# Kernel optimization log

Measured on AMD Instinct MI355X. Metric: run time of the kernel, lower is better.

## Reference

```python
import jax, jax.numpy as jnp
import numpy as np

N_PIX = 596   # (151-2)*(6-2) after two VALID 2x2 convs
HEADS, D = 4, 64

def _ln(x, axes, g=None, b=None, eps=1e-5):
    mu = jnp.mean(x, axes, keepdims=True)
    var = jnp.var(x, axes, keepdims=True)
    y = (x - mu) * jax.lax.rsqrt(var + eps)
    return y * g + b if g is not None else y

def _conv(x, w, b):
    y = jax.lax.conv_general_dilated(x, w, (1, 1), 'VALID',
                                     dimension_numbers=('NCHW', 'OIHW', 'NCHW'))
    return y + b[None, :, None, None]


def setup_inputs() -> dict:
    key = jax.random.key(0)
    ks = jax.random.split(key, 24)
    f32 = jnp.float32
    w = lambda k, s: jax.random.normal(k, s, f32) * 0.05
    inp = {
        'x': jax.random.normal(ks[0], (64, 4, 151, 6), f32),
        'conv1_w': w(ks[1], (16, 4, 2, 2)),  'conv1_b': w(ks[2], (16,)),
        'conv2_w': w(ks[3], (32, 16, 2, 2)), 'conv2_b': w(ks[4], (32,)),
        'kp_w': w(ks[5], (34, 256)),  'kp_b': w(ks[6], (256,)),
        'qp_w': w(ks[7], (34, 256)),  'qp_b': w(ks[8], (256,)),
        'vp_w': w(ks[9], (34, 256)),  'vp_b': w(ks[10], (256,)),
        'klin_w': w(ks[11], (64, N_PIX)), 'klin_b': w(ks[12], (N_PIX,)),
        'qlin_w': w(ks[13], (64, N_PIX)), 'qlin_b': w(ks[14], (N_PIX,)),
        'alin_w': w(ks[15], (N_PIX, N_PIX)), 'alin_b': w(ks[16], (N_PIX,)),
        'knorm_g': jnp.ones((HEADS, N_PIX, D), f32), 'knorm_b': jnp.zeros((HEADS, N_PIX, D), f32),
        'qnorm_g': jnp.ones((HEADS, N_PIX, D), f32), 'qnorm_b': jnp.zeros((HEADS, N_PIX, D), f32),
        'vnorm_g': jnp.ones((HEADS, N_PIX, D), f32), 'vnorm_b': jnp.zeros((HEADS, N_PIX, D), f32),
        'lin1_w': w(ks[17], (256, 64)), 'lin1_b': w(ks[18], (64,)),
        'lin2_w': w(ks[19], (64, 10)),  'lin2_b': w(ks[20], (10,)),
    }
    return inp


def reference(x, conv1_w, conv1_b, conv2_w, conv2_b,
              kp_w, kp_b, qp_w, qp_b, vp_w, vp_b,
              klin_w, klin_b, qlin_w, qlin_b, alin_w, alin_b,
              knorm_g, knorm_b, qnorm_g, qnorm_b, vnorm_g, vnorm_b,
              lin1_w, lin1_b, lin2_w, lin2_b):
    h = jax.nn.relu(_conv(x, conv1_w, conv1_b))
    h = jax.nn.relu(_conv(h, conv2_w, conv2_b))          # (N,32,149,4)
    N, C, cH, cW = h.shape
    xc = jnp.broadcast_to(jnp.arange(cW, dtype=h.dtype) / cW, (cH, cW))
    yc = jnp.broadcast_to((jnp.arange(cH, dtype=h.dtype) / cH)[:, None], (cH, cW))
    sp = jnp.broadcast_to(jnp.stack([xc, yc])[None], (N, 2, cH, cW))
    feats = jnp.concatenate([h, sp], axis=1).transpose(0, 2, 3, 1).reshape(N, N_PIX, C + 2)
    proj = lambda w_, b_: (feats @ w_ + b_).reshape(N, N_PIX, HEADS, D).transpose(0, 2, 1, 3)
    K = _ln(proj(kp_w, kp_b), (1, 2, 3), knorm_g, knorm_b)   # (N,h,596,64)
    Q = _ln(proj(qp_w, qp_b), (1, 2, 3), qnorm_g, qnorm_b)
    V = _ln(proj(vp_w, vp_b), (1, 2, 3), vnorm_g, vnorm_b)
    A = jax.nn.elu((Q @ qlin_w + qlin_b) + (K @ klin_w + klin_b))  # (N,h,596,596)
    A = jax.nn.softmax(A @ alin_w + alin_b, axis=-1)
    E = jnp.einsum('bhfc,bhcd->bhfd', A, V)                  # (N,h,596,64)
    E = E.transpose(0, 2, 1, 3).reshape(N, N_PIX, HEADS * D)
    E = jax.nn.relu(E @ lin1_w + lin1_b)
    E = _ln(E, (1, 2))                                       # LN over [596,64], no affine
    E = jnp.max(E, axis=1)                                   # (N,64)
    return jax.nn.elu(E @ lin2_w + lin2_b)                   # (N,10)
```

## Files before the change

### kernel.cpp

```cpp
#include <hip/hip_runtime.h>
#include <hip/hip_bf16.h>
#include <math.h>

typedef __hip_bfloat16 bf16;
typedef unsigned short ushort;
typedef __attribute__((ext_vector_type(8))) short short8;
typedef __attribute__((ext_vector_type(4))) float float4v;

#define BATCH 64
#define NPIX 596
#define CH 34
#define PC 256

static __device__ __forceinline__ ushort f2bu(float v){ bf16 h = __float2bfloat16(v); return *(ushort*)&h; }
static __device__ __forceinline__ float bu2f(ushort u){ bf16 h = *(bf16*)&u; return __bfloat162float(h); }
static __device__ __forceinline__ float eluf(float x){ return x > 0.f ? x : expm1f(x); }

__global__ __launch_bounds__(256) void k_conv_feats(
    const float* __restrict__ x,
    const float* __restrict__ w1, const float* __restrict__ b1,
    const float* __restrict__ w2, const float* __restrict__ b2,
    ushort* __restrict__ featsH, ushort* __restrict__ featsL)
{
  __shared__ float sw1[256];
  __shared__ float sb1[16];
  __shared__ float sw2[2048];
  __shared__ float sb2[32];
  __shared__ float h1[16*20*5];
  const int s = blockIdx.x, b = blockIdx.y, t = threadIdx.x;
  const float* xb = x + (size_t)b * 4*151*6;

  const int p0 = s*75;
  const int p1 = (p0+75 < NPIX) ? p0+75 : NPIX;
  const int rA = p0>>2, rB = (p1-1)>>2;
  const int nh = rB - rA + 2;

  sw1[t]=w1[t];
  if (t<16) sb1[t]=b1[t];
  for (int i=t;i<2048;i+=256) sw2[i]=w2[i];
  if (t<32) sb2[t]=b2[t];
  __syncthreads();

  for (int i=t; i<16*nh*5; i+=256){
    int oc = i/(nh*5), rem = i - oc*(nh*5);
    int lr = rem/5, cc = rem - (rem/5)*5;
    int r = rA + lr;
    float acc = sb1[oc];
    #pragma unroll
    for (int ic=0;ic<4;ic++){
      const float* xp = xb + ic*906 + r*6 + cc;
      const float* wp = sw1 + oc*16 + ic*4;
      acc += xp[0]*wp[0] + xp[1]*wp[1] + xp[6]*wp[2] + xp[7]*wp[3];
    }
    h1[(oc*20 + lr)*5 + cc] = fmaxf(acc, 0.f);
  }
  __syncthreads();

  const int np = p1 - p0;
  ushort* fbH = featsH + (size_t)b*NPIX*64;
  ushort* fbL = featsL + (size_t)b*NPIX*64;
  const short8 z8 = {0,0,0,0,0,0,0,0};
  for (int i=t;i<np*4;i+=256){
    int pl = i>>2, off = 32 + (i&3)*8;
    int p = p0 + pl;
    *(short8*)(fbH + (size_t)p*64 + off) = z8;
    *(short8*)(fbL + (size_t)p*64 + off) = z8;
  }
  for (int i=t;i<32*np;i+=256){
    int oc = i/np, pl = i - oc*np;
    int p = p0 + pl;
    int r = p>>2, cc = p&3;
    int lr = r - rA;
    float acc = sb2[oc];
    #pragma unroll
    for (int ic=0;ic<16;ic++){
      const float* hp = h1 + (ic*20 + lr)*5 + cc;
      const float* wp = sw2 + oc*64 + ic*4;
      acc += hp[0]*wp[0] + hp[1]*wp[1] + hp[5]*wp[2] + hp[6]*wp[3];
    }
    float v = fmaxf(acc, 0.f);
    ushort hu = f2bu(v);
    fbH[(size_t)p*64+oc] = hu;
    fbL[(size_t)p*64+oc] = f2bu(v - bu2f(hu));
  }
  __syncthreads();
  for (int pl=t; pl<np; pl+=256){
    int p = p0 + pl;
    float v1 = (float)(p&3)*0.25f;
    float v2 = (float)(p>>2)*(1.0f/149.0f);
    ushort h1u = f2bu(v1), h2u = f2bu(v2);
    fbH[(size_t)p*64+32] = h1u;  fbL[(size_t)p*64+32] = f2bu(v1 - bu2f(h1u));
    fbH[(size_t)p*64+33] = h2u;  fbL[(size_t)p*64+33] = f2bu(v2 - bu2f(h2u));
  }
}

__global__ __launch_bounds__(256) void k_prep(
    const float* __restrict__ aw, const float* __restrict__ qw, const float* __restrict__ kw,
    const float* __restrict__ l1w,
    const float* __restrict__ kpw, const float* __restrict__ qpw, const float* __restrict__ vpw,
    ushort* __restrict__ alinP, ushort* __restrict__ WqkP, ushort* __restrict__ w1T,
    ushort* __restrict__ projP)
{
  __shared__ float sA[4][32][17];
  const int t = threadIdx.x, w = t>>6, l = t&63;
  const int gw = blockIdx.x*4 + w;

  if (gw < 1016){
    const float* src; ushort* dst;
    int row0, col0, nrow, ncol, rstride; size_t slot;
    if (gw < 760){
      int tile = gw/19, kk = gw - tile*19;
      src = aw; rstride = NPIX; nrow = NPIX; ncol = NPIX;
      row0 = kk*32; col0 = tile*16;
      dst = alinP; slot = (size_t)gw*64;
    } else if (gw < 920){
      int g1 = gw - 760;
      int tile = g1>>2, kk = g1&3;
      rstride = NPIX; nrow = 64; ncol = NPIX;
      col0 = tile*16;
      if (kk < 2){ src = qw; row0 = kk*32; }
      else       { src = kw; row0 = (kk-2)*32; }
      dst = WqkP; slot = (size_t)g1*64;
    } else {
      int g2 = gw - 920;
      int which = g2>>5, rem = g2&31;
      int tile = rem>>1, kk = rem&1;
      src = which==0 ? kpw : which==1 ? qpw : vpw;
      rstride = PC; nrow = CH; ncol = PC;
      row0 = kk*32; col0 = tile*16;
      dst = projP; slot = (size_t)g2*64;
    }
    #pragma unroll
    for (int p=0;p<2;p++){
      int rr = p*16 + (l>>2);
      int r = row0 + rr;
      int cb = (l&3)*4;
      #pragma unroll
      for (int j=0;j<4;j++){
        int c = col0 + cb + j;
        float v = (r < nrow && c < ncol) ? src[(size_t)r*rstride + c] : 0.f;
        sA[w][rr][cb + j] = v;
      }
    }
    __syncthreads();
    int nloc = l&15, c0 = (l>>4)*8;
    ushort out[8];
    #pragma unroll
    for (int i=0;i<8;i++) out[i] = f2bu(sA[w][c0+i][nloc]);
    *(short8*)(dst + (slot + l)*8) = *(short8*)out;
  } else {
    int s3 = (gw - 1016)*64 + l;
    int n = s3>>5, e0 = (s3&31)*8;
    ushort out[8];
    #pragma unroll
    for (int i=0;i<8;i++) out[i] = f2bu(l1w[(size_t)(e0+i)*64 + n]);
    *(short8*)(w1T + (size_t)s3*8) = *(short8*)out;
  }
}

__global__ __launch_bounds__(256) void k_proj_p1(
    const ushort* __restrict__ featsH, const ushort* __restrict__ featsL,
    const ushort* __restrict__ projP,
    const float* __restrict__ kpb, const float* __restrict__ qpb, const float* __restrict__ vpb,
    float* __restrict__ statsP)
{
  __shared__ float red[8];
  const int rb = blockIdx.x, b = blockIdx.y, which = blockIdx.z;
  const int t = threadIdx.x, w = t>>6, l = t&63, quad = l>>4, ln = l&15;
  const float* Bv = which==0 ? kpb : which==1 ? qpb : vpb;

  float4v acc[4][4];
  #pragma unroll
  for (int ms=0;ms<4;ms++)
    #pragma unroll
    for (int i=0;i<4;i++) acc[ms][i] = (float4v){0.f,0.f,0.f,0.f};

  #pragma unroll
  for (int kk=0;kk<4;kk++){
    const ushort* fb = (kk<2 ? featsH : featsL) + (size_t)b*NPIX*64;
    short8 aq[4];
    #pragma unroll
    for (int ms=0;ms<4;ms++){
      int r = rb*64 + ms*16 + ln;
      short8 z = {0,0,0,0,0,0,0,0};
      aq[ms] = (r < NPIX) ? *(const short8*)(fb + (size_t)r*64 + (kk&1)*32 + quad*8) : z;
    }
    #pragma unroll
    for (int i=0;i<4;i++){
      int tile = w + 4*i;
      short8 bf = *(const short8*)(projP + ((size_t)((which*16 + tile)*2 + (kk&1))*64 + l)*8);
      #pragma unroll
      for (int ms=0;ms<4;ms++)
        acc[ms][i] = __builtin_amdgcn_mfma_f32_16x16x32_bf16(aq[ms], bf, acc[ms][i], 0,0,0);
    }
  }
  float s=0.f, s2=0.f;
  #pragma unroll
  for (int i=0;i<4;i++){
    int col = (w+4*i)*16 + ln;
    float bc = Bv[col];
    #pragma unroll
    for (int ms=0;ms<4;ms++)
      #pragma unroll
      for (int r=0;r<4;r++){
        int p = rb*64 + ms*16 + quad*4 + r;
        if (p < NPIX){
          float v = acc[ms][i][r] + bc;
          s += v; s2 += v*v;
        }
      }
  }
  #pragma unroll
  for (int o=32;o>0;o>>=1){ s += __shfl_down(s,o); s2 += __shfl_down(s2,o); }
  if (l==0){ red[w]=s; red[4+w]=s2; }
  __syncthreads();
  if (t==0){
    atomicAdd(&statsP[(which*64+b)*2],   red[0]+red[1]+red[2]+red[3]);
    atomicAdd(&statsP[(which*64+b)*2+1], red[4]+red[5]+red[6]+red[7]);
  }
}

__global__ __launch_bounds__(256) void k_proj_p2(
    const ushort* __restrict__ featsH, const ushort* __restrict__ featsL,
    const ushort* __restrict__ projP,
    const float* __restrict__ kpb, const float* __restrict__ qpb, const float* __restrict__ vpb,
    const float* __restrict__ kg, const float* __restrict__ kb_,
    const float* __restrict__ qg, const float* __restrict__ qb_,
    const float* __restrict__ vg, const float* __restrict__ vb_,
    const float* __restrict__ statsP,
    ushort* __restrict__ Kb, ushort* __restrict__ Qb, ushort* __restrict__ VP)
{
  __shared__ ushort vtile[64*264];
  const int rb = blockIdx.x, b = blockIdx.y, which = blockIdx.z;
  const int t = threadIdx.x, w = t>>6, l = t&63, quad = l>>4, ln = l&15;
  const float* Bv = which==0 ? kpb : which==1 ? qpb : vpb;
  const float* G  = which==0 ? kg  : which==1 ? qg  : vg;
  const float* Be = which==0 ? kb_ : which==1 ? qb_ : vb_;

  float4v acc[4][4];
  #pragma unroll
  for (int ms=0;ms<4;ms++)
    #pragma unroll
    for (int i=0;i<4;i++) acc[ms][i] = (float4v){0.f,0.f,0.f,0.f};

  #pragma unroll
  for (int kk=0;kk<4;kk++){
    const ushort* fb = (kk<2 ? featsH : featsL) + (size_t)b*NPIX*64;
    short8 aq[4];
    #pragma unroll
    for (int ms=0;ms<4;ms++){
      int r = rb*64 + ms*16 + ln;
      short8 z = {0,0,0,0,0,0,0,0};
      aq[ms] = (r < NPIX) ? *(const short8*)(fb + (size_t)r*64 + (kk&1)*32 + quad*8) : z;
    }
    #pragma unroll
    for (int i=0;i<4;i++){
      int tile = w + 4*i;
      short8 bf = *(const short8*)(projP + ((size_t)((which*16 + tile)*2 + (kk&1))*64 + l)*8);
      #pragma unroll
      for (int ms=0;ms<4;ms++)
        acc[ms][i] = __builtin_amdgcn_mfma_f32_16x16x32_bf16(aq[ms], bf, acc[ms][i], 0,0,0);
    }
  }
  const float n = (float)(NPIX*PC);
  const float S  = statsP[(which*64+b)*2];
  const float S2 = statsP[(which*64+b)*2+1];
  const float mu = S/n;
  const float rs = rsqrtf(S2/n - mu*mu + 1e-5f);

  if (which < 2){
    ushort* out = which==0 ? Kb : Qb;
    #pragma unroll
    for (int i=0;i<4;i++){
      int col = (w+4*i)*16 + ln;
      int h = col>>6, d = col&63;
      float bc = Bv[col];
      #pragma unroll
      for (int ms=0;ms<4;ms++)
        #pragma unroll
        for (int r=0;r<4;r++){
          int p = rb*64 + ms*16 + quad*4 + r;
          if (p < NPIX){
            int gi = (h*NPIX+p)*64 + d;
            float y = (acc[ms][i][r] + bc - mu)*rs*G[gi] + Be[gi];
            out[((size_t)(b*4+h)*NPIX + p)*64 + d] = f2bu(y);
          }
        }
    }
  } else {
    #pragma unroll
    for (int i=0;i<4;i++){
      int col = (w+4*i)*16 + ln;
      int h = col>>6, d = col&63;
      float bc = Bv[col];
      #pragma unroll
      for (int ms=0;ms<4;ms++)
        #pragma unroll
        for (int r=0;r<4;r++){
          int lrow = ms*16 + quad*4 + r;
          int p = rb*64 + lrow;
          ushort o = 0;
          if (p < NPIX){
            int gi = (h*NPIX+p)*64 + d;
            o = f2bu((acc[ms][i][r] + bc - mu)*rs*G[gi] + Be[gi]);
          }
          vtile[lrow*264 + col] = o;
        }
    }
    __syncthreads();
    #pragma unroll
    for (int e=0;e<8;e++){
      int sid = e*256 + t;
      int l2 = sid & 63;
      int rest = sid >> 6;
      int kkL = rest & 1, w2 = (rest>>1)&3, hh = rest>>3;
      int kk = rb*2 + kkL;
      if (kk < 19){
        int lrow0 = kkL*32 + ((l2>>4)<<3);
        int col = hh*64 + w2*16 + (l2&15);
        ushort o[8];
        #pragma unroll
        for (int jj=0;jj<8;jj++) o[jj] = vtile[(lrow0+jj)*264 + col];
        *(short8*)(VP + ((size_t)(b*4+hh)*4864 + (w2*19 + kk)*64 + l2)*8) = *(short8*)o;
      }
    }
  }
}

__global__ __launch_bounds__(512, 2) void k_attn(
    const ushort* __restrict__ Qb, const ushort* __restrict__ Kb,
    const ushort* __restrict__ alinP, const ushort* __restrict__ WqkP,
    const ushort* __restrict__ VP,
    const float* __restrict__ qbias, const float* __restrict__ kbias,
    const float* __restrict__ abias,
    ushort* __restrict__ Ew)
{
  extern __shared__ __align__(16) ushort sm[];
  ushort* strip = sm;
  float*  red   = (float*)(sm + 78848);
  float*  rsum  = (float*)(sm + 78848 + 2048);

  const int t = threadIdx.x;
  const int w = t>>6, l = t&63, quad = l>>4, ln = l&15;
  const int id  = blockIdx.x + blockIdx.y*5;
  const int xcd = id & 7, idx = id >> 3;
  const int lin = xcd*160 + idx;
  const int bh  = lin/5, rb = lin - bh*5;
  const int b = bh>>2, h = bh&3;
  const int row0 = rb*128;
  const ushort* Qp = Qb + (size_t)bh*NPIX*64;
  const ushort* Kp = Kb + (size_t)bh*NPIX*64;

  float4v acc[8][5];
  #pragma unroll
  for (int ms=0;ms<8;ms++)
    #pragma unroll
    for (int i=0;i<5;i++) acc[ms][i] = (float4v){0.f,0.f,0.f,0.f};

  #pragma unroll
  for (int kk=0;kk<4;kk++){
    short8 aq[8];
    #pragma unroll
    for (int ms=0;ms<8;ms++){
      int r = row0 + ms*16 + ln;
      short8 z = {0,0,0,0,0,0,0,0};
      aq[ms] = (r < NPIX)
        ? *(const short8*)((kk<2 ? Qp : Kp) + (size_t)r*64 + (kk&1)*32 + quad*8) : z;
    }
    __builtin_amdgcn_s_setprio(1);
    #pragma unroll
    for (int i=0;i<5;i++){
      int tile = w + 8*i;
      short8 bf = *(const short8*)(WqkP + ((size_t)(tile*4 + kk)*64 + l)*8);
      #pragma unroll
      for (int ms=0;ms<8;ms++)
        acc[ms][i] = __builtin_amdgcn_mfma_f32_16x16x32_bf16(aq[ms], bf, acc[ms][i], 0,0,0);
    }
    __builtin_amdgcn_s_setprio(0);
  }
  #pragma unroll
  for (int i=0;i<5;i++){
    int t0 = w + 8*i;
    if (t0 < 38){
      int col = t0*16 + ln;
      bool cv = col < NPIX;
      float qkb = cv ? (qbias[col] + kbias[col]) : 0.f;
      #pragma unroll
      for (int ms=0;ms<8;ms++)
        #pragma unroll
        for (int r=0;r<4;r++){
          float v = 0.f;
          if (cv){ float xx = acc[ms][i][r] + qkb; v = xx > 0.f ? xx : __expf(xx) - 1.f; }
          strip[(ms*16+quad*4+r)*616 + col] = f2bu(v);
        }
    }
  }
  __syncthreads();

  #pragma unroll
  for (int ms=0;ms<8;ms++)
    #pragma unroll
    for (int i=0;i<5;i++) acc[ms][i] = (float4v){0.f,0.f,0.f,0.f};
  for (int kk=0;kk<19;kk++){
    short8 af[8];
    #pragma unroll
    for (int ms=0;ms<8;ms++)
      af[ms] = *(const short8*)(strip + (ms*16+ln)*616 + kk*32 + quad*8);
    __builtin_amdgcn_s_setprio(1);
    #pragma unroll
    for (int i=0;i<5;i++){
      int tile = w + 8*i;
      short8 bf = *(const short8*)(alinP + ((size_t)(tile*19 + kk)*64 + l)*8);
      #pragma unroll
      for (int ms=0;ms<8;ms++)
        acc[ms][i] = __builtin_amdgcn_mfma_f32_16x16x32_bf16(af[ms], bf, acc[ms][i], 0,0,0);
    }
    __builtin_amdgcn_s_setprio(0);
  }
  __syncthreads();

  float sum[8][4];
  #pragma unroll
  for (int ms=0;ms<8;ms++)
    #pragma unroll
    for (int r=0;r<4;r++) sum[ms][r] = 0.f;
  #pragma unroll
  for (int i=0;i<5;i++){
    int t0 = w + 8*i;
    if (t0 < 38){
      int col = t0*16 + ln;
      bool cv = col < NPIX;
      float ab = cv ? abias[col] : 0.f;
      #pragma unroll
      for (int ms=0;ms<8;ms++)
        #pragma unroll
        for (int r=0;r<4;r++){
          float e = cv ? __expf(acc[ms][i][r] + ab) : 0.f;
          sum[ms][r] += e;
          strip[(ms*16+quad*4+r)*616 + col] = f2bu(e);
        }
    }
  }
  #pragma unroll
  for (int ms=0;ms<8;ms++)
    #pragma unroll
    for (int r=0;r<4;r++)
      #pragma unroll
      for (int o=8;o>0;o>>=1) sum[ms][r] += __shfl_xor(sum[ms][r], o, 16);
  if (ln==0){
    #pragma unroll
    for (int ms=0;ms<8;ms++)
      #pragma unroll
      for (int r=0;r<4;r++) red[(ms*16+quad*4+r)*8 + w] = sum[ms][r];
  }
  __syncthreads();
  if (t < 128){
    float4v v0 = *(float4v*)&red[t*8];
    float4v v1 = *(float4v*)&red[t*8+4];
    rsum[t] = (v0[0]+v0[1]+v0[2]+v0[3]) + (v1[0]+v1[1]+v1[2]+v1[3]);
  }
  __syncthreads();

  const int wr = w>>2, wc = w&3;
  float4v ve[4];
  #pragma unroll
  for (int ms=0;ms<4;ms++) ve[ms] = (float4v){0.f,0.f,0.f,0.f};
  for (int kk=0;kk<19;kk++){
    short8 bf = *(const short8*)(VP + ((size_t)bh*4864 + (wc*19 + kk)*64 + l)*8);
    __builtin_amdgcn_s_setprio(1);
    #pragma unroll
    for (int ms=0;ms<4;ms++){
      short8 af = *(const short8*)(strip + (wr*64 + ms*16+ln)*616 + kk*32 + quad*8);
      ve[ms] = __builtin_amdgcn_mfma_f32_16x16x32_bf16(af, bf, ve[ms], 0,0,0);
    }
    __builtin_amdgcn_s_setprio(0);
  }
  #pragma unroll
  for (int ms=0;ms<4;ms++)
    #pragma unroll
    for (int r=0;r<4;r++){
      int lrow = wr*64 + ms*16 + quad*4 + r;
      int p = row0 + lrow;
      if (p < NPIX){
        float inv = 1.f / rsum[lrow];
        Ew[((size_t)b*NPIX + p)*256 + h*64 + wc*16 + ln] = f2bu(ve[ms][r] * inv);
      }
    }
}

__global__ __launch_bounds__(256) void k_lin1(
    const ushort* __restrict__ Ew, const ushort* __restrict__ w1T,
    const float* __restrict__ bias,
    float* __restrict__ colmax, float* __restrict__ stats)
{
  __shared__ ushort sw1[64*264];
  __shared__ float red[8];
  const int t = threadIdx.x;
  const int w = t>>6, l = t&63, quad = l>>4, ln = l&15;
  const int rb = blockIdx.x, b = blockIdx.y;
  for (int g=t; g<2048; g+=256){
    int row = g>>5, q = g&31;
    *(short8*)(sw1 + row*264 + q*8) = *(const short8*)(w1T + row*256 + q*8);
  }
  __syncthreads();
  float4v acc[4];
  #pragma unroll
  for (int ms=0;ms<4;ms++) acc[ms] = (float4v){0.f,0.f,0.f,0.f};
  #pragma unroll
  for (int kk=0;kk<8;kk++){
    short8 bf = *(const short8*)(sw1 + (w*16+ln)*264 + kk*32 + quad*8);
    #pragma unroll
    for (int ms=0;ms<4;ms++){
      int p = rb*64 + ms*16 + ln;
      size_t rowi = (size_t)b*NPIX + (p < NPIX ? p : 0);
      short8 a = *(const short8*)(Ew + rowi*256 + kk*32 + quad*8);
      acc[ms] = __builtin_amdgcn_mfma_f32_16x16x32_bf16(a, bf, acc[ms], 0,0,0);
    }
  }
  const int col = w*16 + ln;
  const float bc = bias[col];
  float s=0.f, s2=0.f, cmx=0.f;
  #pragma unroll
  for (int ms=0;ms<4;ms++)
    #pragma unroll
    for (int r=0;r<4;r++){
      int p = rb*64 + ms*16 + quad*4 + r;
      if (p < NPIX){
        float v = fmaxf(acc[ms][r] + bc, 0.f);
        s += v; s2 += v*v;
        cmx = fmaxf(cmx, v);
      }
    }
  cmx = fmaxf(cmx, __shfl_xor(cmx, 16, 64));
  cmx = fmaxf(cmx, __shfl_xor(cmx, 32, 64));
  if (quad == 0)
    atomicMax((int*)&colmax[b*64 + col], __float_as_int(cmx));
  #pragma unroll
  for (int o=32;o>0;o>>=1){ s += __shfl_down(s,o); s2 += __shfl_down(s2,o); }
  if (l==0){ red[w]=s; red[4+w]=s2; }
  __syncthreads();
  if (t==0){
    atomicAdd(&stats[b*2],   red[0]+red[1]+red[2]+red[3]);
    atomicAdd(&stats[b*2+1], red[4]+red[5]+red[6]+red[7]);
  }
}

__global__ __launch_bounds__(64) void k_final(
    const float* __restrict__ colmax, const float* __restrict__ stats,
    const float* __restrict__ w2, const float* __restrict__ b2v,
    float* __restrict__ out)
{
  __shared__ float nm[64];
  const int b = blockIdx.x, t = threadIdx.x;
  {
    float mm = colmax[b*64 + t];
    const float n = (float)(NPIX*64);
    float S = stats[b*2], S2 = stats[b*2+1];
    float mu = S/n, var = S2/n - mu*mu;
    nm[t] = (mm - mu) * rsqrtf(var + 1e-5f);
  }
  __syncthreads();
  if (t<10){
    float acc = b2v[t];
    for (int e=0;e<64;e++) acc += nm[e]*w2[e*10+t];
    out[b*10+t] = eluf(acc);
  }
}

extern "C" void kernel_launch(void* const* d_in, const int* in_sizes, int n_in,
                              void* d_out, int out_size, void* d_ws, size_t ws_size,
                              hipStream_t stream)
{
  const float* x       = (const float*)d_in[0];
  const float* conv1_w = (const float*)d_in[1];
  const float* conv1_b = (const float*)d_in[2];
  const float* conv2_w = (const float*)d_in[3];
  const float* conv2_b = (const float*)d_in[4];
  const float* kp_w    = (const float*)d_in[5];
  const float* kp_b    = (const float*)d_in[6];
  const float* qp_w    = (const float*)d_in[7];
  const float* qp_b    = (const float*)d_in[8];
  const float* vp_w    = (const float*)d_in[9];
  const float* vp_b    = (const float*)d_in[10];
  const float* klin_w  = (const float*)d_in[11];
  const float* klin_b  = (const float*)d_in[12];
  const float* qlin_w  = (const float*)d_in[13];
  const float* qlin_b  = (const float*)d_in[14];
  const float* alin_w  = (const float*)d_in[15];
  const float* alin_b  = (const float*)d_in[16];
  const float* knorm_g = (const float*)d_in[17];
  const float* knorm_b = (const float*)d_in[18];
  const float* qnorm_g = (const float*)d_in[19];
  const float* qnorm_b = (const float*)d_in[20];
  const float* vnorm_g = (const float*)d_in[21];
  const float* vnorm_b = (const float*)d_in[22];
  const float* lin1_w  = (const float*)d_in[23];
  const float* lin1_b  = (const float*)d_in[24];
  const float* lin2_w  = (const float*)d_in[25];
  const float* lin2_b  = (const float*)d_in[26];

  float* feats  = (float*)d_ws;
  float* F      = feats + (size_t)BATCH*NPIX*CH;
  float* statsE = F + (size_t)BATCH*NPIX*64;
  float* statsP = statsE + 128;
  float* colmax = statsP + 384;
  ushort* Qb    = (ushort*)(colmax + 4096);
  ushort* Kb    = Qb + (size_t)BATCH*4*NPIX*64;
  ushort* Vb    = Kb + (size_t)BATCH*4*NPIX*64;
  ushort* Ew    = Vb + (size_t)BATCH*4*NPIX*64;
  ushort* w1T   = Ew + (size_t)BATCH*NPIX*256;
  ushort* alinP = w1T + 16384;
  ushort* WqkP  = alinP + 389120;
  ushort* VP    = WqkP + 81920;
  ushort* projP = VP + 9961472;
  ushort* featsH = (ushort*)feats;
  ushort* featsL = (ushort*)F;

  hipMemsetAsync(statsE, 0, 4608*sizeof(float), stream);

  dim3 gc(8, BATCH);
  k_conv_feats<<<gc, 256, 0, stream>>>(x, conv1_w, conv1_b, conv2_w, conv2_b, featsH, featsL);

  k_prep<<<262, 256, 0, stream>>>(alin_w, qlin_w, klin_w, lin1_w, kp_w, qp_w, vp_w,
                                  alinP, WqkP, w1T, projP);

  dim3 gp(10, BATCH, 3);
  k_proj_p1<<<gp, 256, 0, stream>>>(featsH, featsL, projP, kp_b, qp_b, vp_b, statsP);
  k_proj_p2<<<gp, 256, 0, stream>>>(featsH, featsL, projP, kp_b, qp_b, vp_b,
                                    knorm_g, knorm_b, qnorm_g, qnorm_b, vnorm_g, vnorm_b,
                                    statsP, Kb, Qb, VP);

  static bool attr_set = false;
  if (!attr_set){
    hipFuncSetAttribute((const void*)k_attn, hipFuncAttributeMaxDynamicSharedMemorySize, 162304);
    attr_set = true;
  }

  dim3 ga(5, BATCH*4);
  k_attn<<<ga, 512, 162304, stream>>>(Qb, Kb, alinP, WqkP, VP,
                                      qlin_b, klin_b, alin_b, Ew);

  dim3 gl(10, BATCH);
  k_lin1<<<gl, 256, 0, stream>>>(Ew, w1T, lin1_b, colmax, statsE);

  k_final<<<BATCH, 64, 0, stream>>>(colmax, statsE, lin2_w, lin2_b, (float*)d_out);
}
```

Before: 523.7 us.

## Compute projection LayerNorm stats via feature Gram matrix instead of extra GEMM pass

Removes the first projection pass that recomputed the full 596x256 projections only to get sum and sum-of-squares for LayerNorm. Instead the conv kernel accumulates a per-batch 34x34 Gram matrix and feature sums, a few extra prep blocks compute W^T W, weight row sums and bias terms, and a small kernel combines them into the mean and variance statistics. This trades a GEMM-sized pass for tiny reductions. The risk is fp32 cancellation in the variance formula and extra atomics in the conv kernel.

```diff
diff --git a/kernel.cpp b/kernel.cpp
--- a/kernel.cpp
+++ b/kernel.cpp
@@ -20,13 +20,15 @@
     const float* __restrict__ x,
     const float* __restrict__ w1, const float* __restrict__ b1,
     const float* __restrict__ w2, const float* __restrict__ b2,
-    ushort* __restrict__ featsH, ushort* __restrict__ featsL)
+    ushort* __restrict__ featsH, ushort* __restrict__ featsL,
+    float* __restrict__ Gbuf, float* __restrict__ sfb)
 {
   __shared__ float sw1[256];
   __shared__ float sb1[16];
   __shared__ float sw2[2048];
   __shared__ float sb2[32];
   __shared__ float h1[16*20*5];
+  __shared__ float fle[75*34];
   const int s = blockIdx.x, b = blockIdx.y, t = threadIdx.x;
   const float* xb = x + (size_t)b * 4*151*6;
 
@@ -82,8 +84,8 @@
     ushort hu = f2bu(v);
     fbH[(size_t)p*64+oc] = hu;
     fbL[(size_t)p*64+oc] = f2bu(v - bu2f(hu));
-  }
-  __syncthreads();
+    fle[pl*34+oc] = v;
+  }
   for (int pl=t; pl<np; pl+=256){
     int p = p0 + pl;
     float v1 = (float)(p&3)*0.25f;
@@ -91,6 +93,20 @@
     ushort h1u = f2bu(v1), h2u = f2bu(v2);
     fbH[(size_t)p*64+32] = h1u;  fbL[(size_t)p*64+32] = f2bu(v1 - bu2f(h1u));
     fbH[(size_t)p*64+33] = h2u;  fbL[(size_t)p*64+33] = f2bu(v2 - bu2f(h2u));
+    fle[pl*34+32] = v1;
+    fle[pl*34+33] = v2;
+  }
+  __syncthreads();
+  for (int i=t;i<1156;i+=256){
+    int e = i/34, e2 = i - e*34;
+    float g = 0.f;
+    for (int pl=0;pl<np;pl++) g += fle[pl*34+e]*fle[pl*34+e2];
+    atomicAdd(&Gbuf[b*1156+i], g);
+  }
+  if (t<34){
+    float sv = 0.f;
+    for (int pl=0;pl<np;pl++) sv += fle[pl*34+t];
+    atomicAdd(&sfb[b*34+t], sv);
   }
 }
 
@@ -98,12 +114,51 @@
     const float* __restrict__ aw, const float* __restrict__ qw, const float* __restrict__ kw,
     const float* __restrict__ l1w,
     const float* __restrict__ kpw, const float* __restrict__ qpw, const float* __restrict__ vpw,
+    const float* __restrict__ kpb, const float* __restrict__ qpb, const float* __restrict__ vpb,
     ushort* __restrict__ alinP, ushort* __restrict__ WqkP, ushort* __restrict__ w1T,
-    ushort* __restrict__ projP)
-{
-  __shared__ float sA[4][32][17];
+    ushort* __restrict__ projP, float* __restrict__ wstats)
+{
+  __shared__ float shm[8704];
   const int t = threadIdx.x, w = t>>6, l = t&63;
+
+  if (blockIdx.x >= 262){
+    const int which = blockIdx.x - 262;
+    const float* W  = which==0 ? kpw : which==1 ? qpw : vpw;
+    const float* Bv = which==0 ? kpb : which==1 ? qpb : vpb;
+    for (int i=t;i<8704;i+=256) shm[i] = W[i];
+    __syncthreads();
+    float* out = wstats + which*1232;
+    for (int i=t;i<1156;i+=256){
+      int e = i/34, e2 = i - e*34;
+      const float4* A = (const float4*)&shm[e*256];
+      const float4* B = (const float4*)&shm[e2*256];
+      float d = 0.f;
+      #pragma unroll 8
+      for (int k2=0;k2<64;k2++){
+        float4 a = A[k2], bb = B[k2];
+        d += a.x*bb.x + a.y*bb.y + a.z*bb.z + a.w*bb.w;
+      }
+      out[i] = d;
+    }
+    if (t < 34){
+      float ws = 0.f, wb = 0.f;
+      for (int c=0;c<256;c++){ float wv = shm[t*256+c]; ws += wv; wb += wv*Bv[c]; }
+      out[1156+t] = ws;
+      out[1190+t] = wb;
+    } else if (t == 34){
+      float sb = 0.f;
+      for (int c=0;c<256;c++) sb += Bv[c];
+      out[1224] = sb;
+    } else if (t == 35){
+      float sb2 = 0.f;
+      for (int c=0;c<256;c++){ float bv = Bv[c]; sb2 += bv*bv; }
+      out[1225] = sb2;
+    }
+    return;
+  }
+
   const int gw = blockIdx.x*4 + w;
+  #define SA(W_,R_,C_) shm[(W_)*544 + (R_)*17 + (C_)]
 
   if (gw < 1016){
     const float* src; ushort* dst;
@@ -139,14 +194,14 @@
       for (int j=0;j<4;j++){
         int c = col0 + cb + j;
         float v = (r < nrow && c < ncol) ? src[(size_t)r*rstride + c] : 0.f;
-        sA[w][rr][cb + j] = v;
+        SA(w, rr, cb+j) = v;
       }
     }
     __syncthreads();
     int nloc = l&15, c0 = (l>>4)*8;
     ushort out[8];
     #pragma unroll
-    for (int i=0;i<8;i++) out[i] = f2bu(sA[w][c0+i][nloc]);
+    for (int i=0;i<8;i++) out[i] = f2bu(SA(w, c0+i, nloc));
     *(short8*)(dst + (slot + l)*8) = *(short8*)out;
   } else {
     int s3 = (gw - 1016)*64 + l;
@@ -156,67 +211,55 @@
     for (int i=0;i<8;i++) out[i] = f2bu(l1w[(size_t)(e0+i)*64 + n]);
     *(short8*)(w1T + (size_t)s3*8) = *(short8*)out;
   }
-}
-
-__global__ __launch_bounds__(256) void k_proj_p1(
-    const ushort* __restrict__ featsH, const ushort* __restrict__ featsL,
-    const ushort* __restrict__ projP,
-    const float* __restrict__ kpb, const float* __restrict__ qpb, const float* __restrict__ vpb,
-    float* __restrict__ statsP)
-{
-  __shared__ float red[8];
-  const int rb = blockIdx.x, b = blockIdx.y, which = blockIdx.z;
-  const int t = threadIdx.x, w = t>>6, l = t&63, quad = l>>4, ln = l&15;
-  const float* Bv = which==0 ? kpb : which==1 ? qpb : vpb;
-
-  float4v acc[4][4];
-  #pragma unroll
-  for (int ms=0;ms<4;ms++)
-    #pragma unroll
-    for (int i=0;i<4;i++) acc[ms][i] = (float4v){0.f,0.f,0.f,0.f};
-
-  #pragma unroll
-  for (int kk=0;kk<4;kk++){
-    const ushort* fb = (kk<2 ? featsH : featsL) + (size_t)b*NPIX*64;
-    short8 aq[4];
-    #pragma unroll
-    for (int ms=0;ms<4;ms++){
-      int r = rb*64 + ms*16 + ln;
-      short8 z = {0,0,0,0,0,0,0,0};
-      aq[ms] = (r < NPIX) ? *(const short8*)(fb + (size_t)r*64 + (kk&1)*32 + quad*8) : z;
-    }
-    #pragma unroll
-    for (int i=0;i<4;i++){
-      int tile = w + 4*i;
-      short8 bf = *(const short8*)(projP + ((size_t)((which*16 + tile)*2 + (kk&1))*64 + l)*8);
-      #pragma unroll
-      for (int ms=0;ms<4;ms++)
-        acc[ms][i] = __builtin_amdgcn_mfma_f32_16x16x32_bf16(aq[ms], bf, acc[ms][i], 0,0,0);
-    }
-  }
-  float s=0.f, s2=0.f;
-  #pragma unroll
-  for (int i=0;i<4;i++){
-    int col = (w+4*i)*16 + ln;
-    float bc = Bv[col];
-    #pragma unroll
-    for (int ms=0;ms<4;ms++)
-      #pragma unroll
-      for (int r=0;r<4;r++){
-        int p = rb*64 + ms*16 + quad*4 + r;
-        if (p < NPIX){
-          float v = acc[ms][i][r] + bc;
-          s += v; s2 += v*v;
-        }
-      }
-  }
-  #pragma unroll
-  for (int o=32;o>0;o>>=1){ s += __shfl_down(s,o); s2 += __shfl_down(s2,o); }
-  if (l==0){ red[w]=s; red[4+w]=s2; }
-  __syncthreads();
-  if (t==0){
-    atomicAdd(&statsP[(which*64+b)*2],   red[0]+red[1]+red[2]+red[3]);
-    atomicAdd(&statsP[(which*64+b)*2+1], red[4]+red[5]+red[6]+red[7]);
+  #undef SA
+}
+
+__global__ __launch_bounds__(256) void k_statsA(
+    const float* __restrict__ Gbuf, const float* __restrict__ sfb,
+    const float* __restrict__ wstats, float* __restrict__ statsP)
+{
+  __shared__ float red[36];
+  const int b = blockIdx.x, t = threadIdx.x, l = t&63, wv = t>>6;
+  float q[3] = {0.f,0.f,0.f};
+  for (int i=t;i<1156;i+=256){
+    float g = Gbuf[b*1156+i];
+    #pragma unroll
+    for (int w2=0;w2<3;w2++) q[w2] += wstats[w2*1232+i]*g;
+  }
+  float d1[3] = {0.f,0.f,0.f}, d2[3] = {0.f,0.f,0.f};
+  if (t < 34){
+    float sv = sfb[b*34+t];
+    #pragma unroll
+    for (int w2=0;w2<3;w2++){
+      d1[w2] = sv*wstats[w2*1232+1156+t];
+      d2[w2] = sv*wstats[w2*1232+1190+t];
+    }
+  }
+  #pragma unroll
+  for (int w2=0;w2<3;w2++)
+    #pragma unroll
+    for (int o=32;o>0;o>>=1){
+      q[w2]  += __shfl_down(q[w2],  o);
+      d1[w2] += __shfl_down(d1[w2], o);
+      d2[w2] += __shfl_down(d2[w2], o);
+    }
+  if (l==0){
+    #pragma unroll
+    for (int w2=0;w2<3;w2++){
+      red[(w2*3+0)*4+wv] = q[w2];
+      red[(w2*3+1)*4+wv] = d1[w2];
+      red[(w2*3+2)*4+wv] = d2[w2];
+    }
+  }
+  __syncthreads();
+  if (t < 3){
+    float Q  = red[(t*3+0)*4] + red[(t*3+0)*4+1] + red[(t*3+0)*4+2] + red[(t*3+0)*4+3];
+    float D1 = red[(t*3+1)*4] + red[(t*3+1)*4+1] + red[(t*3+1)*4+2] + red[(t*3+1)*4+3];
+    float D2 = red[(t*3+2)*4] + red[(t*3+2)*4+1] + red[(t*3+2)*4+2] + red[(t*3+2)*4+3];
+    float Sb  = wstats[t*1232+1224];
+    float Sb2 = wstats[t*1232+1225];
+    statsP[(t*64+b)*2]   = D1 + (float)NPIX*Sb;
+    statsP[(t*64+b)*2+1] = Q + 2.f*D2 + (float)NPIX*Sb2;
   }
 }
 
@@ -604,7 +647,10 @@
   float* statsE = F + (size_t)BATCH*NPIX*64;
   float* statsP = statsE + 128;
   float* colmax = statsP + 384;
-  ushort* Qb    = (ushort*)(colmax + 4096);
+  float* Gbuf   = colmax + 4096;
+  float* sfb    = Gbuf + 73984;
+  float* wstats = sfb + 2176;
+  ushort* Qb    = (ushort*)(wstats + 3696);
   ushort* Kb    = Qb + (size_t)BATCH*4*NPIX*64;
   ushort* Vb    = Kb + (size_t)BATCH*4*NPIX*64;
   ushort* Ew    = Vb + (size_t)BATCH*4*NPIX*64;
@@ -616,16 +662,19 @@
   ushort* featsH = (ushort*)feats;
   ushort* featsL = (ushort*)F;
 
-  hipMemsetAsync(statsE, 0, 4608*sizeof(float), stream);
+  hipMemsetAsync(statsE, 0, 80768*sizeof(float), stream);
 
   dim3 gc(8, BATCH);
-  k_conv_feats<<<gc, 256, 0, stream>>>(x, conv1_w, conv1_b, conv2_w, conv2_b, featsH, featsL);
-
-  k_prep<<<262, 256, 0, stream>>>(alin_w, qlin_w, klin_w, lin1_w, kp_w, qp_w, vp_w,
-                                  alinP, WqkP, w1T, projP);
+  k_conv_feats<<<gc, 256, 0, stream>>>(x, conv1_w, conv1_b, conv2_w, conv2_b,
+                                       featsH, featsL, Gbuf, sfb);
+
+  k_prep<<<265, 256, 0, stream>>>(alin_w, qlin_w, klin_w, lin1_w, kp_w, qp_w, vp_w,
+                                  kp_b, qp_b, vp_b,
+                                  alinP, WqkP, w1T, projP, wstats);
+
+  k_statsA<<<BATCH, 256, 0, stream>>>(Gbuf, sfb, wstats, statsP);
 
   dim3 gp(10, BATCH, 3);
-  k_proj_p1<<<gp, 256, 0, stream>>>(featsH, featsL, projP, kp_b, qp_b, vp_b, statsP);
   k_proj_p2<<<gp, 256, 0, stream>>>(featsH, featsL, projP, kp_b, qp_b, vp_b,
                                     knorm_g, knorm_b, qnorm_g, qnorm_b, vnorm_g, vnorm_b,
                                     statsP, Kb, Qb, VP);
```

Result: slower. 567.6 us (+8.4%).
